# Kernel optimization log

Hardware: AMD Instinct MI355X
Metric: run time of the kernel (lower is better)

The kernel has to match this reference:

```python
import jax, jax.numpy as jnp
import numpy as np

N = 50000   # nodes
E = 600000  # edges per relation
F = 256     # dim_features
H = 128     # dim_hiddens == dim_embs
Q = 64      # dim_query
R = 2       # relations per sign (etypes)
L = 2       # conv_depth


def setup_inputs() -> dict:
    key = jax.random.key(0)
    ks = jax.random.split(key, 11)
    s = 0.05
    return {
        "x_attr": jax.random.normal(ks[0], (N, F), jnp.float32),
        "x_stru": jax.random.normal(ks[1], (N, F), jnp.float32),
        # edges_*: [sign(pos/neg), relation, (src,dst), E]
        "edges_attr": jax.random.randint(ks[2], (2, R, 2, E), 0, N),
        "edges_stru": jax.random.randint(ks[3], (2, R, 2, E), 0, N),
        # params, leading dim 2 = (pos_emb_model, neg_emb_model)
        "Wf": jax.random.normal(ks[4], (2, H, F), jnp.float32) * s,
        "convW": jax.random.normal(ks[5], (2, L, R, H, H), jnp.float32) * s,
        "convB": jnp.zeros((2, L, R, H), jnp.float32),
        "attnW1": jax.random.normal(ks[6], (2, L, H, Q), jnp.float32) * s,
        "attnB1": jnp.zeros((2, L, Q), jnp.float32),
        "attnW2": jax.random.normal(ks[7], (2, L, Q), jnp.float32) * s,
        "Wc": jax.random.normal(ks[8], (2, H, 3 * H), jnp.float32) * s,
    }


def _gcn(h, src, dst, W, b):
    """DGL GraphConv, norm='both', degrees clamped to >=1."""
    n = h.shape[0]
    ones = jnp.ones(src.shape[0], h.dtype)
    deg_out = jnp.clip(jax.ops.segment_sum(ones, src, num_segments=n), 1.0)
    deg_in = jnp.clip(jax.ops.segment_sum(ones, dst, num_segments=n), 1.0)
    m = (h * (deg_out ** -0.5)[:, None]) @ W          # (N, H)
    agg = jax.ops.segment_sum(m[src], dst, num_segments=n)  # gather-scatter over edges
    return agg * (deg_in ** -0.5)[:, None] + b


def _het_layer(h, edges, Ws, bs, W1, b1, w2):
    """HeteroGraphConv with per-node attention aggregation over relations.
    edges: (R, 2, E); Ws: (R,H,H); bs: (R,H)."""
    hs = jnp.stack([_gcn(h, edges[r, 0], edges[r, 1], Ws[r], bs[r]) for r in range(R)])  # (R,N,H)
    scores = jnp.einsum('rnq,q->rn', jnp.tanh(jnp.einsum('rnd,dq->rnq', hs, W1) + b1), w2)
    a = jax.nn.softmax(scores, axis=0)                # (R,N) attention over relations
    return jnp.einsum('rn,rnd->nd', a, hs), a


def _hetattn(x, edges, Wf, cW, cB, aW1, aB1, aW2, Wc):
    h0 = jnp.tanh(x @ Wf.T)                                        # (N,H)
    h1, _ = _het_layer(h0, edges, cW[1], cB[1], aW1[1], aB1[1], aW2[1])   # 1-hop via last conv
    hA, _ = _het_layer(h0, edges, cW[0], cB[0], aW1[0], aB1[0], aW2[0])
    h2, attn = _het_layer(hA, edges, cW[1], cB[1], aW1[1], aB1[1], aW2[1])  # 2-hop
    y = jnp.concatenate([h0, h1, h2], axis=-1) @ Wc.T              # concat_weight
    return y, attn.T


def reference(x_attr, x_stru, edges_attr, edges_stru, Wf, convW, convB,
              attnW1, attnB1, attnW2, Wc):
    def run(sign, x, edges):
        y, _ = _hetattn(x, edges[sign], Wf[sign], convW[sign], convB[sign],
                        attnW1[sign], attnB1[sign], attnW2[sign], Wc[sign])
        return y
    embs_attr_pos = run(0, x_attr, edges_attr)
    embs_stru_pos = run(0, x_stru, edges_stru)
    embs_attr_neg = run(1, x_attr, edges_attr)
    embs_stru_neg = run(1, x_stru, edges_stru)
    return (embs_attr_pos, embs_stru_pos, embs_attr_neg, embs_stru_neg)
```

## Files before the change

### kernel.cpp

```cpp
#include <hip/hip_runtime.h>
#include <math.h>

constexpr int N_ = 50000;
constexpr int E_ = 600000;
constexpr int F_ = 256;
constexpr int H_ = 128;
constexpr int Q_ = 64;
constexpr int R_ = 2;
constexpr int L_ = 2;

#define MODE_STORE 0
#define MODE_TANH  1
#define MODE_ACC   2

template <bool BT>
__global__ __launch_bounds__(256) void gemm_kernel(
    const float* __restrict__ A, int lda,
    const float* __restrict__ B, int ldb,
    float* __restrict__ C, int ldc,
    int M, int K,
    const float* __restrict__ rowscale, int mode)
{
    __shared__ __align__(16) float As[16][68];
    __shared__ __align__(16) float Bs[16][132];

    const int row0 = blockIdx.x * 64;
    const int col0 = blockIdx.y * 128;
    const int tid  = threadIdx.x;
    const int tm = tid >> 4;
    const int tn = tid & 15;

    float acc[4][8] = {};

    for (int kk = 0; kk < K; kk += 16) {
        {
            const int m  = tid >> 2;
            const int k4 = (tid & 3) * 4;
            const int r  = row0 + m;
            float4 v = make_float4(0.f, 0.f, 0.f, 0.f);
            if (r < M) v = *(const float4*)(A + (size_t)r * lda + kk + k4);
            As[k4 + 0][m] = v.x; As[k4 + 1][m] = v.y;
            As[k4 + 2][m] = v.z; As[k4 + 3][m] = v.w;
        }
        if (BT) {
            const int j  = tid >> 1;
            const int k8 = (tid & 1) * 8;
            const float* bp = B + (size_t)(col0 + j) * ldb + kk + k8;
            float4 v0 = *(const float4*)(bp);
            float4 v1 = *(const float4*)(bp + 4);
            Bs[k8 + 0][j] = v0.x; Bs[k8 + 1][j] = v0.y;
            Bs[k8 + 2][j] = v0.z; Bs[k8 + 3][j] = v0.w;
            Bs[k8 + 4][j] = v1.x; Bs[k8 + 5][j] = v1.y;
            Bs[k8 + 6][j] = v1.z; Bs[k8 + 7][j] = v1.w;
        } else {
            const int k  = tid >> 5;
            const int j4 = (tid & 31) * 4;
            float4 v0 = *(const float4*)(B + (size_t)(kk + k) * ldb + col0 + j4);
            float4 v1 = *(const float4*)(B + (size_t)(kk + k + 8) * ldb + col0 + j4);
            Bs[k + 0][j4 + 0] = v0.x; Bs[k + 0][j4 + 1] = v0.y;
            Bs[k + 0][j4 + 2] = v0.z; Bs[k + 0][j4 + 3] = v0.w;
            Bs[k + 8][j4 + 0] = v1.x; Bs[k + 8][j4 + 1] = v1.y;
            Bs[k + 8][j4 + 2] = v1.z; Bs[k + 8][j4 + 3] = v1.w;
        }
        __syncthreads();

        #pragma unroll
        for (int k = 0; k < 16; k++) {
            const float4 av  = *(const float4*)&As[k][tm * 4];
            const float4 bv0 = *(const float4*)&Bs[k][tn * 8];
            const float4 bv1 = *(const float4*)&Bs[k][tn * 8 + 4];
            const float a[4] = {av.x, av.y, av.z, av.w};
            const float b[8] = {bv0.x, bv0.y, bv0.z, bv0.w,
                                bv1.x, bv1.y, bv1.z, bv1.w};
            #pragma unroll
            for (int i = 0; i < 4; i++)
                #pragma unroll
                for (int j = 0; j < 8; j++)
                    acc[i][j] += a[i] * b[j];
        }
        __syncthreads();
    }

    #pragma unroll
    for (int i = 0; i < 4; i++) {
        const int r = row0 + tm * 4 + i;
        if (r >= M) continue;
        const float rs = rowscale ? rowscale[r] : 1.0f;
        #pragma unroll
        for (int j = 0; j < 8; j++) {
            const int c = col0 + tn * 8 + j;
            float v = acc[i][j] * rs;
            if (mode == MODE_TANH) v = tanhf(v);
            float* p = C + (size_t)r * ldc + c;
            if (mode == MODE_ACC) *p += v;
            else                  *p = v;
        }
    }
}

__global__ __launch_bounds__(256) void gemm_conv_pair(
    const float* __restrict__ A, int lda,
    const float* __restrict__ B0, const float* __restrict__ B1,
    float* __restrict__ C0, float* __restrict__ C1,
    int M, const float* __restrict__ rs0, const float* __restrict__ rs1)
{
    __shared__ __align__(16) float As[16][68];
    __shared__ __align__(16) float B0s[16][68];
    __shared__ __align__(16) float B1s[16][68];

    const int row0 = blockIdx.x * 64;
    const int col0 = blockIdx.y * 64;
    const int tid  = threadIdx.x;
    const int tm = tid >> 4;
    const int tn = tid & 15;

    float acc0[4][4] = {};
    float acc1[4][4] = {};

    for (int kk = 0; kk < H_; kk += 16) {
        {
            const int m  = tid >> 2;
            const int k4 = (tid & 3) * 4;
            const int r  = row0 + m;
            float4 v = make_float4(0.f, 0.f, 0.f, 0.f);
            if (r < M) v = *(const float4*)(A + (size_t)r * lda + kk + k4);
            As[k4 + 0][m] = v.x; As[k4 + 1][m] = v.y;
            As[k4 + 2][m] = v.z; As[k4 + 3][m] = v.w;
        }
        {
            const int k  = tid >> 4;
            const int j4 = (tid & 15) * 4;
            float4 v0 = *(const float4*)(B0 + (size_t)(kk + k) * H_ + col0 + j4);
            float4 v1 = *(const float4*)(B1 + (size_t)(kk + k) * H_ + col0 + j4);
            B0s[k][j4 + 0] = v0.x; B0s[k][j4 + 1] = v0.y;
            B0s[k][j4 + 2] = v0.z; B0s[k][j4 + 3] = v0.w;
            B1s[k][j4 + 0] = v1.x; B1s[k][j4 + 1] = v1.y;
            B1s[k][j4 + 2] = v1.z; B1s[k][j4 + 3] = v1.w;
        }
        __syncthreads();

        #pragma unroll
        for (int k = 0; k < 16; k++) {
            const float4 av  = *(const float4*)&As[k][tm * 4];
            const float4 bv0 = *(const float4*)&B0s[k][tn * 4];
            const float4 bv1 = *(const float4*)&B1s[k][tn * 4];
            const float a[4]  = {av.x, av.y, av.z, av.w};
            const float b0[4] = {bv0.x, bv0.y, bv0.z, bv0.w};
            const float b1v[4] = {bv1.x, bv1.y, bv1.z, bv1.w};
            #pragma unroll
            for (int i = 0; i < 4; i++)
                #pragma unroll
                for (int j = 0; j < 4; j++) {
                    acc0[i][j] += a[i] * b0[j];
                    acc1[i][j] += a[i] * b1v[j];
                }
        }
        __syncthreads();
    }

    #pragma unroll
    for (int i = 0; i < 4; i++) {
        const int r = row0 + tm * 4 + i;
        if (r >= M) continue;
        const float s0 = rs0[r];
        const float s1 = rs1[r];
        #pragma unroll
        for (int j = 0; j < 4; j++) {
            const int c = col0 + tn * 4 + j;
            C0[(size_t)r * H_ + c] = acc0[i][j] * s0;
            C1[(size_t)r * H_ + c] = acc1[i][j] * s1;
        }
    }
}

__global__ __launch_bounds__(256) void zero_i(int* __restrict__ p, int n)
{
    int t = blockIdx.x * 256 + threadIdx.x;
    if (t < n) p[t] = 0;
}

__global__ __launch_bounds__(256) void count_deg(const int* __restrict__ eb,
                                                 int* __restrict__ cnt, int total)
{
    int t = blockIdx.x * 256 + threadIdx.x;
    if (t >= total) return;
    int which = t / E_;
    atomicAdd(&cnt[which * N_ + eb[t]], 1);
}

__global__ __launch_bounds__(256) void deg_finalize(const int* __restrict__ cnt,
                                                    float* __restrict__ dscale, int n)
{
    int t = blockIdx.x * 256 + threadIdx.x;
    if (t < n) {
        int v = cnt[t];
        dscale[t] = rsqrtf((float)(v < 1 ? 1 : v));
    }
}

constexpr int SCAN_NB = (N_ + 255) / 256;

__global__ __launch_bounds__(256) void scan_p1(const int* __restrict__ cnt,
                                               int* __restrict__ bsums)
{
    const int r = blockIdx.y;
    const int* in = cnt + (size_t)(2 * r + 1) * N_;
    const int i = blockIdx.x * 256 + threadIdx.x;
    int v = (i < N_) ? in[i] : 0;
    #pragma unroll
    for (int off = 32; off > 0; off >>= 1) v += __shfl_xor(v, off);
    __shared__ int ws[4];
    if ((threadIdx.x & 63) == 0) ws[threadIdx.x >> 6] = v;
    __syncthreads();
    if (threadIdx.x == 0)
        bsums[r * SCAN_NB + blockIdx.x] = ws[0] + ws[1] + ws[2] + ws[3];
}

__global__ __launch_bounds__(256) void scan_p2(int* __restrict__ bsums)
{
    __shared__ int sh[256];
    const int r = blockIdx.x;
    const int t = threadIdx.x;
    int v = (t < SCAN_NB) ? bsums[r * SCAN_NB + t] : 0;
    sh[t] = v;
    __syncthreads();
    #pragma unroll
    for (int d = 1; d < 256; d <<= 1) {
        int u = (t >= d) ? sh[t - d] : 0;
        __syncthreads();
        sh[t] += u;
        __syncthreads();
    }
    if (t < SCAN_NB) bsums[r * SCAN_NB + t] = sh[t] - v;
}

__global__ __launch_bounds__(256) void scan_p3(const int* __restrict__ cnt,
                                               const int* __restrict__ bsums,
                                               int* __restrict__ offs,
                                               int* __restrict__ cursor)
{
    __shared__ int sh[256];
    const int r = blockIdx.y;
    const int* in = cnt + (size_t)(2 * r + 1) * N_;
    int* out = offs + (size_t)r * (N_ + 1);
    int* cur = cursor + (size_t)r * N_;
    const int i = blockIdx.x * 256 + threadIdx.x;
    const int t = threadIdx.x;
    int v = (i < N_) ? in[i] : 0;
    sh[t] = v;
    __syncthreads();
    #pragma unroll
    for (int d = 1; d < 256; d <<= 1) {
        int u = (t >= d) ? sh[t - d] : 0;
        __syncthreads();
        sh[t] += u;
        __syncthreads();
    }
    const int excl = sh[t] - v + bsums[r * SCAN_NB + blockIdx.x];
    if (i < N_) { out[i] = excl; cur[i] = excl; }
    if (i == 0) out[N_] = E_;
}

__global__ __launch_bounds__(256) void csr_fill(const int* __restrict__ eb,
                                                int* __restrict__ cursor,
                                                int* __restrict__ csr, int total)
{
    int t = blockIdx.x * 256 + threadIdx.x;
    if (t >= total) return;
    int r = (t >= E_) ? 1 : 0;
    int e = t - r * E_;
    int s = eb[(r * 2 + 0) * E_ + e];
    int d = eb[(r * 2 + 1) * E_ + e];
    int pos = atomicAdd(&cursor[r * N_ + d], 1);
    csr[(size_t)r * E_ + pos] = s;
}

__device__ __forceinline__ void gather_rel(const float2* __restrict__ m,
                                           const int* __restrict__ csr,
                                           int b, int e, int lane, float2& acc)
{
    int k = b;
    for (; k + 8 <= e; k += 8) {
        int s[8];
        #pragma unroll
        for (int u = 0; u < 8; u++) s[u] = csr[k + u];
        float2 v[8];
        #pragma unroll
        for (int u = 0; u < 8; u++) v[u] = m[(size_t)s[u] * 64 + lane];
        #pragma unroll
        for (int u = 0; u < 8; u++) { acc.x += v[u].x; acc.y += v[u].y; }
    }
    if (k + 4 <= e) {
        const int s0 = csr[k + 0];
        const int s1 = csr[k + 1];
        const int s2 = csr[k + 2];
        const int s3 = csr[k + 3];
        const float2 v0 = m[(size_t)s0 * 64 + lane];
        const float2 v1 = m[(size_t)s1 * 64 + lane];
        const float2 v2 = m[(size_t)s2 * 64 + lane];
        const float2 v3 = m[(size_t)s3 * 64 + lane];
        acc.x += (v0.x + v1.x) + (v2.x + v3.x);
        acc.y += (v0.y + v1.y) + (v2.y + v3.y);
        k += 4;
    }
    for (; k < e; k++) {
        const int s = csr[k];
        const float2 v = m[(size_t)s * 64 + lane];
        acc.x += v.x; acc.y += v.y;
    }
}

__global__ __launch_bounds__(1024, 8) void pull_attn(
    const float2* __restrict__ m0, const float2* __restrict__ m1,
    const int* __restrict__ offs0, const int* __restrict__ csr0,
    const int* __restrict__ offs1, const int* __restrict__ csr1,
    const float* __restrict__ si0, const float* __restrict__ si1,
    const float* __restrict__ bias0, const float* __restrict__ bias1,
    const float* __restrict__ W1, const float* __restrict__ b1,
    const float* __restrict__ w2, float2* __restrict__ outb, int n)
{
    __shared__ float W1s[H_ * Q_];
    __shared__ float2 hsS[16][2][Q_];
    __shared__ float b1s[Q_], w2s[Q_], bAs[H_], bBs[H_];

    for (int i = threadIdx.x; i < H_ * Q_; i += 1024) W1s[i] = W1[i];
    if (threadIdx.x < Q_) { b1s[threadIdx.x] = b1[threadIdx.x]; w2s[threadIdx.x] = w2[threadIdx.x]; }
    {
        const int t = (int)threadIdx.x - Q_;
        if (t >= 0 && t < H_) bAs[t] = bias0[t];
        const int u = (int)threadIdx.x - Q_ - H_;
        if (u >= 0 && u < H_) bBs[u] = bias1[u];
    }
    __syncthreads();

    const int lane = threadIdx.x & 63;
    const int wv   = threadIdx.x >> 6;
    int node = (blockIdx.x * 1024 + threadIdx.x) >> 6;
    node = __builtin_amdgcn_readfirstlane(node);

    float2 hs0 = make_float2(0.f, 0.f), hs1 = hs0;

    if (node < n) {
        float2 a0 = make_float2(0.f, 0.f), a1 = a0;
        const int b0  = offs0[node], e0 = offs0[node + 1];
        const int b1i = offs1[node], e1 = offs1[node + 1];
        gather_rel(m0, csr0, b0,  e0, lane, a0);
        gather_rel(m1, csr1, b1i, e1, lane, a1);

        const float sc0 = si0[node], sc1 = si1[node];
        hs0.x = a0.x * sc0 + bAs[2 * lane];
        hs0.y = a0.y * sc0 + bAs[2 * lane + 1];
        hs1.x = a1.x * sc1 + bBs[2 * lane];
        hs1.y = a1.y * sc1 + bBs[2 * lane + 1];
        hsS[wv][0][lane] = hs0;
        hsS[wv][1][lane] = hs1;
    }

    __asm__ volatile("s_waitcnt lgkmcnt(0)" ::: "memory");
    __builtin_amdgcn_sched_barrier(0);

    if (node < n) {
        const float* h0p = (const float*)&hsS[wv][0][0];
        const float* h1p = (const float*)&hsS[wv][1][0];
        float t0 = b1s[lane], t1 = b1s[lane];
        #pragma unroll 8
        for (int i = 0; i < H_; i++) {
            const float wval = W1s[i * Q_ + lane];
            t0 += h0p[i] * wval;
            t1 += h1p[i] * wval;
        }
        float s0 = tanhf(t0) * w2s[lane];
        float s1 = tanhf(t1) * w2s[lane];
        #pragma unroll
        for (int off = 32; off > 0; off >>= 1) {
            s0 += __shfl_xor(s0, off);
            s1 += __shfl_xor(s1, off);
        }
        const float mx = fmaxf(s0, s1);
        const float e0v = expf(s0 - mx), e1v = expf(s1 - mx);
        const float a0 = e0v / (e0v + e1v), a1 = 1.0f - a0;

        float2 o;
        o.x = a0 * hs0.x + a1 * hs1.x;
        o.y = a0 * hs0.y + a1 * hs1.y;
        outb[(size_t)node * 64 + lane] = o;
    }
}

extern "C" void kernel_launch(void* const* d_in, const int* in_sizes, int n_in,
                              void* d_out, int out_size, void* d_ws, size_t ws_size,
                              hipStream_t stream)
{
    const float* x_attr = (const float*)d_in[0];
    const float* x_stru = (const float*)d_in[1];
    const int*   e_attr = (const int*)d_in[2];
    const int*   e_stru = (const int*)d_in[3];
    const float* Wf     = (const float*)d_in[4];
    const float* convW  = (const float*)d_in[5];
    const float* convB  = (const float*)d_in[6];
    const float* aW1    = (const float*)d_in[7];
    const float* aB1    = (const float*)d_in[8];
    const float* aW2    = (const float*)d_in[9];
    const float* Wc     = (const float*)d_in[10];
    float*       out    = (float*)d_out;
    float*       ws     = (float*)d_ws;

    const size_t NH = (size_t)N_ * H_;
    float* A  = ws;
    float* Bb = ws + 1 * NH;
    float* C  = ws + 2 * NH;
    float* D  = ws + 3 * NH;
    float* dscale = ws + 4 * NH;
    int*   ibase  = (int*)(dscale + 4 * N_);
    int*   cnt    = ibase;
    int*   offs   = ibase + 4 * N_;
    int*   csr    = offs + 2 * (N_ + 1);
    int*   cursor = csr + 2 * E_;
    int*   bsums  = cursor + 2 * N_;

    const int GX = (N_ + 63) / 64;
    const dim3 GGEMM(GX, 1);
    const dim3 GCONV(GX, 2);
    const dim3 GSCAN(SCAN_NB, 2);
    const int PA_B = (N_ * 64) / 1024;

    for (int run = 0; run < 4; run++) {
        const int sign = run >> 1;
        const float* x = (run & 1) ? x_stru : x_attr;
        const int* eb = ((run & 1) ? e_stru : e_attr) + (size_t)sign * (R_ * 2 * E_);
        float* y = out + (size_t)run * NH;
        const float* WcS = Wc + (size_t)sign * H_ * 3 * H_;

        zero_i<<<(4 * N_ + 255) / 256, 256, 0, stream>>>(cnt, 4 * N_);
        count_deg<<<(4 * E_ + 255) / 256, 256, 0, stream>>>(eb, cnt, 4 * E_);
        deg_finalize<<<(4 * N_ + 255) / 256, 256, 0, stream>>>(cnt, dscale, 4 * N_);
        scan_p1<<<GSCAN, 256, 0, stream>>>(cnt, bsums);
        scan_p2<<<2, 256, 0, stream>>>(bsums);
        scan_p3<<<GSCAN, 256, 0, stream>>>(cnt, bsums, offs, cursor);
        csr_fill<<<(2 * E_ + 255) / 256, 256, 0, stream>>>(eb, cursor, csr, 2 * E_);

        gemm_kernel<true><<<GGEMM, 256, 0, stream>>>(
            x, F_, Wf + (size_t)sign * H_ * F_, F_, A, H_, N_, F_, nullptr, MODE_TANH);

        gemm_kernel<true><<<GGEMM, 256, 0, stream>>>(
            A, H_, WcS, 3 * H_, y, H_, N_, H_, nullptr, MODE_STORE);

        auto het = [&](const float* h_in, int l, float* outb) {
            const size_t lo = (size_t)(sign * L_ + l);
            gemm_conv_pair<<<GCONV, 256, 0, stream>>>(
                h_in, H_,
                convW + (lo * R_ + 0) * H_ * H_,
                convW + (lo * R_ + 1) * H_ * H_,
                C, D, N_,
                dscale + 0 * N_, dscale + 2 * N_);
            pull_attn<<<PA_B, 1024, 0, stream>>>(
                (const float2*)C, (const float2*)D,
                offs, csr, offs + (N_ + 1), csr + E_,
                dscale + N_, dscale + 3 * N_,
                convB + (lo * R_ + 0) * H_, convB + (lo * R_ + 1) * H_,
                aW1 + lo * H_ * Q_, aB1 + lo * Q_, aW2 + lo * Q_,
                (float2*)outb, N_);
        };

        het(A, 1, Bb);
        gemm_kernel<true><<<GGEMM, 256, 0, stream>>>(
            Bb, H_, WcS + H_, 3 * H_, y, H_, N_, H_, nullptr, MODE_ACC);

        het(A, 0, Bb);

        het(Bb, 1, A);
        gemm_kernel<true><<<GGEMM, 256, 0, stream>>>(
            A, H_, WcS + 2 * H_, 3 * H_, y, H_, N_, H_, nullptr, MODE_ACC);
    }
}
```

Before: 3.660 ms.

## Double-buffer GEMM shared tiles, shrink gather unroll, vectorize attention LDS reads

Both GEMM kernels now use two shared-memory buffers and prefetch the next K-tile into registers while computing the current one, so each step needs one barrier instead of two and global loads can overlap with FMAs. The edge gather loop drops its 8-way unroll in favour of a 4-way loop, which lowers register pressure in the 1024-thread pull kernel at the cost of fewer loads in flight. The attention score loop reads hidden values from LDS as float4 instead of scalars. The changes touch unrelated kernels, and the doubled shared memory and extra prefetch registers may reduce GEMM occupancy.

```diff
diff --git a/kernel.cpp b/kernel.cpp
--- a/kernel.cpp
+++ b/kernel.cpp
@@ -21,8 +21,8 @@
     int M, int K,
     const float* __restrict__ rowscale, int mode)
 {
-    __shared__ __align__(16) float As[16][68];
-    __shared__ __align__(16) float Bs[16][132];
+    __shared__ __align__(16) float As[2][16][68];
+    __shared__ __align__(16) float Bs[2][16][132];
 
     const int row0 = blockIdx.x * 64;
     const int col0 = blockIdx.y * 128;
@@ -30,45 +30,64 @@
     const int tm = tid >> 4;
     const int tn = tid & 15;
 
+    const int am  = tid >> 2;
+    const int ak4 = (tid & 3) * 4;
+    const int bj  = tid >> 1;
+    const int bk8 = (tid & 1) * 8;
+    const int bk  = tid >> 5;
+    const int bj4 = (tid & 31) * 4;
+
+    auto loadA = [&](int kk) -> float4 {
+        const int r = row0 + am;
+        if (r < M) return *(const float4*)(A + (size_t)r * lda + kk + ak4);
+        return make_float4(0.f, 0.f, 0.f, 0.f);
+    };
+    auto loadB = [&](int kk, float4& v0, float4& v1) {
+        if (BT) {
+            const float* bp = B + (size_t)(col0 + bj) * ldb + kk + bk8;
+            v0 = *(const float4*)(bp);
+            v1 = *(const float4*)(bp + 4);
+        } else {
+            v0 = *(const float4*)(B + (size_t)(kk + bk) * ldb + col0 + bj4);
+            v1 = *(const float4*)(B + (size_t)(kk + bk + 8) * ldb + col0 + bj4);
+        }
+    };
+    auto storeT = [&](int b, float4 va, float4 v0, float4 v1) {
+        As[b][ak4 + 0][am] = va.x; As[b][ak4 + 1][am] = va.y;
+        As[b][ak4 + 2][am] = va.z; As[b][ak4 + 3][am] = va.w;
+        if (BT) {
+            Bs[b][bk8 + 0][bj] = v0.x; Bs[b][bk8 + 1][bj] = v0.y;
+            Bs[b][bk8 + 2][bj] = v0.z; Bs[b][bk8 + 3][bj] = v0.w;
+            Bs[b][bk8 + 4][bj] = v1.x; Bs[b][bk8 + 5][bj] = v1.y;
+            Bs[b][bk8 + 6][bj] = v1.z; Bs[b][bk8 + 7][bj] = v1.w;
+        } else {
+            Bs[b][bk + 0][bj4 + 0] = v0.x; Bs[b][bk + 0][bj4 + 1] = v0.y;
+            Bs[b][bk + 0][bj4 + 2] = v0.z; Bs[b][bk + 0][bj4 + 3] = v0.w;
+            Bs[b][bk + 8][bj4 + 0] = v1.x; Bs[b][bk + 8][bj4 + 1] = v1.y;
+            Bs[b][bk + 8][bj4 + 2] = v1.z; Bs[b][bk + 8][bj4 + 3] = v1.w;
+        }
+    };
+
     float acc[4][8] = {};
 
-    for (int kk = 0; kk < K; kk += 16) {
-        {
-            const int m  = tid >> 2;
-            const int k4 = (tid & 3) * 4;
-            const int r  = row0 + m;
-            float4 v = make_float4(0.f, 0.f, 0.f, 0.f);
-            if (r < M) v = *(const float4*)(A + (size_t)r * lda + kk + k4);
-            As[k4 + 0][m] = v.x; As[k4 + 1][m] = v.y;
-            As[k4 + 2][m] = v.z; As[k4 + 3][m] = v.w;
-        }
-        if (BT) {
-            const int j  = tid >> 1;
-            const int k8 = (tid & 1) * 8;
-            const float* bp = B + (size_t)(col0 + j) * ldb + kk + k8;
-            float4 v0 = *(const float4*)(bp);
-            float4 v1 = *(const float4*)(bp + 4);
-            Bs[k8 + 0][j] = v0.x; Bs[k8 + 1][j] = v0.y;
-            Bs[k8 + 2][j] = v0.z; Bs[k8 + 3][j] = v0.w;
-            Bs[k8 + 4][j] = v1.x; Bs[k8 + 5][j] = v1.y;
-            Bs[k8 + 6][j] = v1.z; Bs[k8 + 7][j] = v1.w;
-        } else {
-            const int k  = tid >> 5;
-            const int j4 = (tid & 31) * 4;
-            float4 v0 = *(const float4*)(B + (size_t)(kk + k) * ldb + col0 + j4);
-            float4 v1 = *(const float4*)(B + (size_t)(kk + k + 8) * ldb + col0 + j4);
-            Bs[k + 0][j4 + 0] = v0.x; Bs[k + 0][j4 + 1] = v0.y;
-            Bs[k + 0][j4 + 2] = v0.z; Bs[k + 0][j4 + 3] = v0.w;
-            Bs[k + 8][j4 + 0] = v1.x; Bs[k + 8][j4 + 1] = v1.y;
-            Bs[k + 8][j4 + 2] = v1.z; Bs[k + 8][j4 + 3] = v1.w;
-        }
-        __syncthreads();
+    {
+        float4 va = loadA(0), v0, v1;
+        loadB(0, v0, v1);
+        storeT(0, va, v0, v1);
+    }
+    __syncthreads();
+
+    int cur = 0;
+    for (int kk = 16; ; kk += 16) {
+        const bool more = (kk < K);
+        float4 na, n0, n1;
+        if (more) { na = loadA(kk); loadB(kk, n0, n1); }
 
         #pragma unroll
         for (int k = 0; k < 16; k++) {
-            const float4 av  = *(const float4*)&As[k][tm * 4];
-            const float4 bv0 = *(const float4*)&Bs[k][tn * 8];
-            const float4 bv1 = *(const float4*)&Bs[k][tn * 8 + 4];
+            const float4 av  = *(const float4*)&As[cur][k][tm * 4];
+            const float4 bv0 = *(const float4*)&Bs[cur][k][tn * 8];
+            const float4 bv1 = *(const float4*)&Bs[cur][k][tn * 8 + 4];
             const float a[4] = {av.x, av.y, av.z, av.w};
             const float b[8] = {bv0.x, bv0.y, bv0.z, bv0.w,
                                 bv1.x, bv1.y, bv1.z, bv1.w};
@@ -78,7 +97,10 @@
                 for (int j = 0; j < 8; j++)
                     acc[i][j] += a[i] * b[j];
         }
+        if (!more) break;
+        storeT(cur ^ 1, na, n0, n1);
         __syncthreads();
+        cur ^= 1;
     }
 
     #pragma unroll
@@ -104,9 +126,9 @@
     float* __restrict__ C0, float* __restrict__ C1,
     int M, const float* __restrict__ rs0, const float* __restrict__ rs1)
 {
-    __shared__ __align__(16) float As[16][68];
-    __shared__ __align__(16) float B0s[16][68];
-    __shared__ __align__(16) float B1s[16][68];
+    __shared__ __align__(16) float As[2][16][68];
+    __shared__ __align__(16) float B0s[2][16][68];
+    __shared__ __align__(16) float B1s[2][16][68];
 
     const int row0 = blockIdx.x * 64;
     const int col0 = blockIdx.y * 64;
@@ -114,36 +136,51 @@
     const int tm = tid >> 4;
     const int tn = tid & 15;
 
+    const int am  = tid >> 2;
+    const int ak4 = (tid & 3) * 4;
+    const int bk  = tid >> 4;
+    const int bj4 = (tid & 15) * 4;
+
+    auto loadA = [&](int kk) -> float4 {
+        const int r = row0 + am;
+        if (r < M) return *(const float4*)(A + (size_t)r * lda + kk + ak4);
+        return make_float4(0.f, 0.f, 0.f, 0.f);
+    };
+    auto storeT = [&](int b, float4 va, float4 v0, float4 v1) {
+        As[b][ak4 + 0][am] = va.x; As[b][ak4 + 1][am] = va.y;
+        As[b][ak4 + 2][am] = va.z; As[b][ak4 + 3][am] = va.w;
+        B0s[b][bk][bj4 + 0] = v0.x; B0s[b][bk][bj4 + 1] = v0.y;
+        B0s[b][bk][bj4 + 2] = v0.z; B0s[b][bk][bj4 + 3] = v0.w;
+        B1s[b][bk][bj4 + 0] = v1.x; B1s[b][bk][bj4 + 1] = v1.y;
+        B1s[b][bk][bj4 + 2] = v1.z; B1s[b][bk][bj4 + 3] = v1.w;
+    };
+
     float acc0[4][4] = {};
     float acc1[4][4] = {};
 
-    for (int kk = 0; kk < H_; kk += 16) {
-        {
-            const int m  = tid >> 2;
-            const int k4 = (tid & 3) * 4;
-            const int r  = row0 + m;
-            float4 v = make_float4(0.f, 0.f, 0.f, 0.f);
-            if (r < M) v = *(const float4*)(A + (size_t)r * lda + kk + k4);
-            As[k4 + 0][m] = v.x; As[k4 + 1][m] = v.y;
-            As[k4 + 2][m] = v.z; As[k4 + 3][m] = v.w;
-        }
-        {
-            const int k  = tid >> 4;
-            const int j4 = (tid & 15) * 4;
-            float4 v0 = *(const float4*)(B0 + (size_t)(kk + k) * H_ + col0 + j4);
-            float4 v1 = *(const float4*)(B1 + (size_t)(kk + k) * H_ + col0 + j4);
-            B0s[k][j4 + 0] = v0.x; B0s[k][j4 + 1] = v0.y;
-            B0s[k][j4 + 2] = v0.z; B0s[k][j4 + 3] = v0.w;
-            B1s[k][j4 + 0] = v1.x; B1s[k][j4 + 1] = v1.y;
-            B1s[k][j4 + 2] = v1.z; B1s[k][j4 + 3] = v1.w;
-        }
-        __syncthreads();
+    {
+        float4 va = loadA(0);
+        float4 v0 = *(const float4*)(B0 + (size_t)bk * H_ + col0 + bj4);
+        float4 v1 = *(const float4*)(B1 + (size_t)bk * H_ + col0 + bj4);
+        storeT(0, va, v0, v1);
+    }
+    __syncthreads();
+
+    int cur = 0;
+    for (int kk = 16; ; kk += 16) {
+        const bool more = (kk < H_);
+        float4 na, n0, n1;
+        if (more) {
+            na = loadA(kk);
+            n0 = *(const float4*)(B0 + (size_t)(kk + bk) * H_ + col0 + bj4);
+            n1 = *(const float4*)(B1 + (size_t)(kk + bk) * H_ + col0 + bj4);
+        }
 
         #pragma unroll
         for (int k = 0; k < 16; k++) {
-            const float4 av  = *(const float4*)&As[k][tm * 4];
-            const float4 bv0 = *(const float4*)&B0s[k][tn * 4];
-            const float4 bv1 = *(const float4*)&B1s[k][tn * 4];
+            const float4 av  = *(const float4*)&As[cur][k][tm * 4];
+            const float4 bv0 = *(const float4*)&B0s[cur][k][tn * 4];
+            const float4 bv1 = *(const float4*)&B1s[cur][k][tn * 4];
             const float a[4]  = {av.x, av.y, av.z, av.w};
             const float b0[4] = {bv0.x, bv0.y, bv0.z, bv0.w};
             const float b1v[4] = {bv1.x, bv1.y, bv1.z, bv1.w};
@@ -155,7 +192,10 @@
                     acc1[i][j] += a[i] * b1v[j];
                 }
         }
+        if (!more) break;
+        storeT(cur ^ 1, na, n0, n1);
         __syncthreads();
+        cur ^= 1;
     }
 
     #pragma unroll
@@ -280,17 +320,7 @@
                                            int b, int e, int lane, float2& acc)
 {
     int k = b;
-    for (; k + 8 <= e; k += 8) {
-        int s[8];
-        #pragma unroll
-        for (int u = 0; u < 8; u++) s[u] = csr[k + u];
-        float2 v[8];
-        #pragma unroll
-        for (int u = 0; u < 8; u++) v[u] = m[(size_t)s[u] * 64 + lane];
-        #pragma unroll
-        for (int u = 0; u < 8; u++) { acc.x += v[u].x; acc.y += v[u].y; }
-    }
-    if (k + 4 <= e) {
+    for (; k + 4 <= e; k += 4) {
         const int s0 = csr[k + 0];
         const int s1 = csr[k + 1];
         const int s2 = csr[k + 2];
@@ -301,7 +331,6 @@
         const float2 v3 = m[(size_t)s3 * 64 + lane];
         acc.x += (v0.x + v1.x) + (v2.x + v3.x);
         acc.y += (v0.y + v1.y) + (v2.y + v3.y);
-        k += 4;
     }
     for (; k < e; k++) {
         const int s = csr[k];
@@ -320,7 +349,7 @@
     const float* __restrict__ w2, float2* __restrict__ outb, int n)
 {
     __shared__ float W1s[H_ * Q_];
-    __shared__ float2 hsS[16][2][Q_];
+    __shared__ __align__(16) float2 hsS[16][2][Q_];
     __shared__ float b1s[Q_], w2s[Q_], bAs[H_], bBs[H_];
 
     for (int i = threadIdx.x; i < H_ * Q_; i += 1024) W1s[i] = W1[i];
@@ -360,14 +389,19 @@
     __builtin_amdgcn_sched_barrier(0);
 
     if (node < n) {
-        const float* h0p = (const float*)&hsS[wv][0][0];
-        const float* h1p = (const float*)&hsS[wv][1][0];
+        const float4* h0p4 = (const float4*)&hsS[wv][0][0];
+        const float4* h1p4 = (const float4*)&hsS[wv][1][0];
         float t0 = b1s[lane], t1 = b1s[lane];
         #pragma unroll 8
-        for (int i = 0; i < H_; i++) {
-            const float wval = W1s[i * Q_ + lane];
-            t0 += h0p[i] * wval;
-            t1 += h1p[i] * wval;
+        for (int i4 = 0; i4 < 32; i4++) {
+            const float4 h0v = h0p4[i4];
+            const float4 h1v = h1p4[i4];
+            const float wa = W1s[(i4 * 4 + 0) * Q_ + lane];
+            const float wb = W1s[(i4 * 4 + 1) * Q_ + lane];
+            const float wc = W1s[(i4 * 4 + 2) * Q_ + lane];
+            const float wd = W1s[(i4 * 4 + 3) * Q_ + lane];
+            t0 += h0v.x * wa + h0v.y * wb + h0v.z * wc + h0v.w * wd;
+            t1 += h1v.x * wa + h1v.y * wb + h1v.z * wc + h1v.w * wd;
         }
         float s0 = tanhf(t0) * w2s[lane];
         float s1 = tanhf(t1) * w2s[lane];
```

After: 3.467 ms. 5.3% less time.
